# Kernel tuning notes

Hardware: AMD Instinct MI355X
Metric: run time of the kernel (lower is better)

The kernel has to match this reference:

```python
import math
import jax, jax.numpy as jnp
import numpy as np

B, T, C = 2, 2048, 1024
N_HEAD = 16
HEAD_DIM = C // N_HEAD


def setup_inputs() -> dict:
    key = jax.random.key(0)
    k1, k2, k3 = jax.random.split(key, 3)
    x = jax.random.normal(k1, (B, T, C), dtype=jnp.float32)
    w_attn = jax.random.normal(k2, (3 * C, C), dtype=jnp.float32) * 0.02
    w_proj = jax.random.normal(k3, (C, C), dtype=jnp.float32) * 0.02
    return {"x": x, "w_attn": w_attn, "w_proj": w_proj}


def _rope_cos_sin(seq_len, dim, dtype):
    inv_freq = 1.0 / (10000.0 ** (jnp.arange(0, dim, 2, dtype=jnp.float32) / dim))
    t = jnp.arange(seq_len, dtype=jnp.float32)
    freqs = jnp.einsum('i,j->ij', t, inv_freq)          # [T, dim/2]
    emb = jnp.concatenate([freqs, freqs], axis=-1)       # [T, dim]
    return jnp.cos(emb).astype(dtype), jnp.sin(emb).astype(dtype)


def _rotate_half(x):
    x1, x2 = jnp.split(x, 2, axis=-1)
    return jnp.concatenate([-x2, x1], axis=-1)


def _apply_rope(x, cos, sin):
    # x: [B, H, T, D]; cos/sin: [T, D] broadcast over batch/head
    return x * cos[None, None] + _rotate_half(x) * sin[None, None]


def reference(x, w_attn, w_proj):
    b, t, c = x.shape
    h, d = N_HEAD, c // N_HEAD
    qkv = x @ w_attn.T                                   # [B, T, 3C]
    q, k, v = jnp.split(qkv, 3, axis=-1)
    q = q.reshape(b, t, h, d).transpose(0, 2, 1, 3)      # [B, H, T, D]
    k = k.reshape(b, t, h, d).transpose(0, 2, 1, 3)
    v = v.reshape(b, t, h, d).transpose(0, 2, 1, 3)
    cos, sin = _rope_cos_sin(t, d, x.dtype)
    q = _apply_rope(q, cos, sin)
    k = _apply_rope(k, cos, sin)
    logits = jnp.einsum('bhqd,bhkd->bhqk', q, k) * (1.0 / math.sqrt(d))
    causal = jnp.tril(jnp.ones((t, t), dtype=bool))
    logits = jnp.where(causal[None, None], logits, jnp.float32(-jnp.inf).astype(logits.dtype))
    att = jax.nn.softmax(logits, axis=-1)                # [B, H, T, T]
    y = jnp.einsum('bhqk,bhkd->bhqd', att, v)            # [B, H, T, D]
    y = y.transpose(0, 2, 1, 3).reshape(b, t, c)
    return y @ w_proj.T
```

## Files before the change

kernel.cpp:

```cpp
#include <hip/hip_runtime.h>
#include <hip/hip_bf16.h>
#include <math.h>

#define B_ 2
#define T_ 2048
#define C_ 1024
#define H_ 16

typedef __bf16 bf16x8 __attribute__((ext_vector_type(8)));
typedef __bf16 bf16x4 __attribute__((ext_vector_type(4)));
typedef float f32x4 __attribute__((ext_vector_type(4)));
typedef float f32x16 __attribute__((ext_vector_type(16)));
typedef unsigned int u32;

#if __has_builtin(__builtin_amdgcn_exp2f)
#define EXP2(x) __builtin_amdgcn_exp2f(x)
#else
#define EXP2(x) exp2f(x)
#endif

__device__ __forceinline__ void gload16(const void* g, void* l) {
    __builtin_amdgcn_global_load_lds(
        (const __attribute__((address_space(1))) void*)g,
        (__attribute__((address_space(3))) void*)l, 16, 0, 0);
}

__device__ __forceinline__ f32x4 mfma16(bf16x8 a, bf16x8 b, f32x4 c) {
    return __builtin_amdgcn_mfma_f32_16x16x32_bf16(a, b, c, 0, 0, 0);
}
__device__ __forceinline__ f32x16 mfma32(bf16x8 a, bf16x8 b, f32x16 c) {
    return __builtin_amdgcn_mfma_f32_32x32x16_bf16(a, b, c, 0, 0, 0);
}

__device__ __forceinline__ u32 cvtpk(float lo, float hi) {
    u32 r;
    asm("v_cvt_pk_bf16_f32 %0, %1, %2" : "=v"(r) : "v"(lo), "v"(hi));
    return r;
}

__device__ __forceinline__ void plane32swap(u32& a, u32& b) {
#if __has_builtin(__builtin_amdgcn_permlane32_swap)
    auto r = __builtin_amdgcn_permlane32_swap(a, b, false, false);
    a = r[0]; b = r[1];
#else
    asm("v_permlane32_swap_b32 %0, %1" : "+v"(a), "+v"(b));
#endif
}

#define SCLQ 0.18033688011112042f
#define NLOG2_10K_32 (-0.4152410118609203f)

__global__ __launch_bounds__(256) void cast_all(const float* __restrict__ x,
                                                const float* __restrict__ wa,
                                                const float* __restrict__ wp,
                                                __bf16* __restrict__ xb,
                                                __bf16* __restrict__ wab,
                                                __bf16* __restrict__ wpb) {
    const int i = blockIdx.x * 256 + threadIdx.x;
    const float* src;
    __bf16* dst;
    int k;
    if (i < 1048576)               { src = x;  dst = xb;  k = i; }
    else if (i < 1048576 + 786432) { src = wa; dst = wab; k = i - 1048576; }
    else                           { src = wp; dst = wpb; k = i - (1048576 + 786432); }
    float4 v = ((const float4*)src)[k];
    bf16x4 o;
    o[0] = (__bf16)v.x; o[1] = (__bf16)v.y; o[2] = (__bf16)v.z; o[3] = (__bf16)v.w;
    ((bf16x4*)dst)[k] = o;
}

__global__ __launch_bounds__(256) void gemm_qkv(const __bf16* __restrict__ A,
                                                const __bf16* __restrict__ Bw,
                                                __bf16* __restrict__ Qb,
                                                __bf16* __restrict__ Kb,
                                                __bf16* __restrict__ Vt) {
    const int tid  = threadIdx.x;
    const int lane = tid & 63;
    const int w    = tid >> 6;
    const int wr = w >> 1, wc = w & 1;
    const int l15 = lane & 15, lg = lane >> 4;
    const int d0  = blockIdx.y * 24 + blockIdx.x;
    const int xcd = d0 & 7, kk0 = d0 >> 3;
    const int by  = xcd * 4 + (kk0 / 24);
    const int bx  = kk0 % 24;
    const int bm = by * 128, bn = bx * 128;
    const int K = C_;
    __shared__ __bf16 Asm[128 * 64];
    __shared__ __bf16 Bsm[128 * 64];
    f32x4 acc[4][4] = {};

    for (int kt = 0; kt < K; kt += 64) {
        if (kt) __syncthreads();
#pragma unroll
        for (int it = 0; it < 4; ++it) {
            const int c = it * 256 + tid;
            const int row = c >> 3, cc = (c & 7) * 8;
            gload16(A  + (size_t)(bm + row) * K + kt + cc, Asm + c * 8);
            gload16(Bw + (size_t)(bn + row) * K + kt + cc, Bsm + c * 8);
        }
        __syncthreads();
#pragma unroll
        for (int kk = 0; kk < 64; kk += 32) {
            bf16x8 af[4], bf[4];
#pragma unroll
            for (int i = 0; i < 4; ++i)
                af[i] = *(const bf16x8*)&Asm[(wr * 64 + i * 16 + l15) * 64 + kk + lg * 8];
#pragma unroll
            for (int j = 0; j < 4; ++j)
                bf[j] = *(const bf16x8*)&Bsm[(wc * 64 + j * 16 + l15) * 64 + kk + lg * 8];
#pragma unroll
            for (int i = 0; i < 4; ++i)
#pragma unroll
                for (int j = 0; j < 4; ++j)
                    acc[i][j] = mfma16(af[i], bf[j], acc[i][j]);
        }
    }
    const int region  = bn >> 10;
    const int colbase = (bn & 1023) + wc * 64;
    const int h = colbase >> 6;
    if (region < 2) {
        __bf16* dst = region ? Kb : Qb;
        const float scl = region ? 1.0f : SCLQ;
#pragma unroll
        for (int j = 0; j < 2; ++j) {
            const int d = j * 16 + l15;
            const float invf = exp2f((float)d * NLOG2_10K_32);
#pragma unroll
            for (int i = 0; i < 4; ++i)
#pragma unroll
                for (int r = 0; r < 4; ++r) {
                    const int row = bm + wr * 64 + i * 16 + lg * 4 + r;
                    const int b = row >> 11, t = row & (T_ - 1);
                    float sv, cv;
                    __sincosf((float)t * invf, &sv, &cv);
                    const float v1 = acc[i][j][r], v2 = acc[i][j + 2][r];
                    const float o1 = (v1 * cv - v2 * sv) * scl;
                    const float o2 = (v2 * cv + v1 * sv) * scl;
                    const size_t base = ((size_t)(b * H_ + h) * T_ + t) * 64;
                    dst[base + d]      = (__bf16)o1;
                    dst[base + d + 32] = (__bf16)o2;
                }
        }
    } else {
#pragma unroll
        for (int i = 0; i < 4; ++i)
#pragma unroll
            for (int j = 0; j < 4; ++j) {
                const int vcol = colbase + j * 16 + l15;
                const int hh = vcol >> 6, d = vcol & 63;
                const int row0 = bm + wr * 64 + i * 16 + lg * 4;
                const int b = row0 >> 11, t0 = row0 & (T_ - 1);
                u32 dw[2];
                dw[0] = cvtpk(acc[i][j][0], acc[i][j][1]);
                dw[1] = cvtpk(acc[i][j][2], acc[i][j][3]);
                *(uint64_t*)&Vt[((size_t)(b * H_ + hh) * 64 + d) * T_ + t0] =
                    *(uint64_t*)dw;
            }
    }
}

__global__ __launch_bounds__(256) void gemm_proj(const __bf16* __restrict__ A,
                                                 const __bf16* __restrict__ Bw,
                                                 float* __restrict__ Cp,
                                                 int N, int K) {
    const int tid  = threadIdx.x;
    const int lane = tid & 63;
    const int w    = tid >> 6;
    const int wr = w >> 1, wc = w & 1;
    const int l15 = lane & 15, lg = lane >> 4;
    const int d0  = blockIdx.y * 8 + blockIdx.x;
    const int xcd = d0 & 7, kk0 = d0 >> 3;
    const int by  = xcd * 8 + (kk0 >> 3);
    const int bx  = kk0 & 7;
    const int bm = by * 64, bn = bx * 128;
    __shared__ __bf16 Asm[64 * 64];
    __shared__ __bf16 Bsm[128 * 64];
    f32x4 acc[2][4] = {};

    for (int kt = 0; kt < K; kt += 64) {
        if (kt) __syncthreads();
#pragma unroll
        for (int it = 0; it < 2; ++it) {
            const int g = it * 256 + tid;
            const int row = g >> 3, cc = (g & 7) * 8;
            gload16(A + (size_t)(bm + row) * K + kt + cc, Asm + g * 8);
        }
#pragma unroll
        for (int it = 0; it < 4; ++it) {
            const int g = it * 256 + tid;
            const int row = g >> 3, cc = (g & 7) * 8;
            gload16(Bw + (size_t)(bn + row) * K + kt + cc, Bsm + g * 8);
        }
        __syncthreads();
#pragma unroll
        for (int kk = 0; kk < 64; kk += 32) {
            bf16x8 af[2], bf[4];
#pragma unroll
            for (int i = 0; i < 2; ++i)
                af[i] = *(const bf16x8*)&Asm[(wr * 32 + i * 16 + l15) * 64 + kk + lg * 8];
#pragma unroll
            for (int j = 0; j < 4; ++j)
                bf[j] = *(const bf16x8*)&Bsm[(wc * 64 + j * 16 + l15) * 64 + kk + lg * 8];
#pragma unroll
            for (int i = 0; i < 2; ++i)
#pragma unroll
                for (int j = 0; j < 4; ++j)
                    acc[i][j] = mfma16(af[i], bf[j], acc[i][j]);
        }
    }
#pragma unroll
    for (int i = 0; i < 2; ++i)
#pragma unroll
        for (int j = 0; j < 4; ++j)
#pragma unroll
            for (int r = 0; r < 4; ++r) {
                const int row = bm + wr * 32 + i * 16 + lg * 4 + r;
                const int col = bn + wc * 64 + j * 16 + l15;
                Cp[(size_t)row * N + col] = acc[i][j][r];
            }
}

__global__ __launch_bounds__(512, 4) void attn_fwd(const __bf16* __restrict__ Qb,
                                                   const __bf16* __restrict__ Kb,
                                                   const __bf16* __restrict__ Vt,
                                                   __bf16* __restrict__ Yatt) {
    const int gid = blockIdx.x;
    const int bh = (gid & 7) * 4 + ((gid >> 3) & 3);
    const int qq = gid >> 5;
    const int qt = (qq < 8) ? (15 - qq) : (qq - 8);
    const int b = bh >> 4, h = bh & 15;
    const int tid = threadIdx.x, lane = tid & 63, w = tid >> 6;
    const int qgrp = w & 3, kvh = w >> 2;
    const int l31 = lane & 31, hi = lane >> 5;
    const int hi4 = hi * 4;
    __shared__ __bf16 Ksm[2][128 * 64];
    __shared__ __bf16 Vsm[2][64 * 128];

    const int Q0 = qt * 128 + qgrp * 32;
    const int qg = Q0 + l31;
    const __bf16* Qp = Qb + ((size_t)bh * T_ + Q0) * 64;
    const __bf16* Kp = Kb + (size_t)bh * T_ * 64;
    const __bf16* Vp = Vt + (size_t)bh * 64 * T_;

    auto STAGE = [&](int j) {
        __bf16* Ks = Ksm[j & 1];
        __bf16* Vs = Vsm[j & 1];
#pragma unroll
        for (int it = 0; it < 2; ++it) {
            const int g = it * 512 + tid;
            const int kr = g >> 3, kc = (g & 7) ^ (kr & 7);
            gload16(Kp + ((size_t)(j * 128 + kr)) * 64 + kc * 8, Ks + g * 8);
            const int vd = g >> 4, vg = (g & 15) ^ (vd & 15);
            gload16(Vp + (size_t)vd * T_ + j * 128 + vg * 8, Vs + g * 8);
        }
    };

    const int jmax = qt + 1;
    STAGE(0);

    bf16x8 qf[4];
#pragma unroll
    for (int ds = 0; ds < 4; ++ds)
        qf[ds] = *(const bf16x8*)&Qp[l31 * 64 + ds * 16 + hi * 8];

    f32x16 ot[2] = {};
    float l_run = 0.f;

    for (int j = 0; j < jmax; ++j) {
        const int cur = j & 1;
        __builtin_amdgcn_s_barrier();
        if (j + 1 < jmax) {
            STAGE(j + 1);
            asm volatile("s_waitcnt vmcnt(4)" ::: "memory");
        } else {
            asm volatile("s_waitcnt vmcnt(0)" ::: "memory");
        }
        __builtin_amdgcn_s_barrier();
        __builtin_amdgcn_sched_barrier(0);

        if (j * 128 + kvh * 64 <= Q0 + 31) {
            f32x16 st[2] = {};
#pragma unroll
            for (int a = 0; a < 2; ++a)
#pragma unroll
                for (int ds = 0; ds < 4; ++ds) {
                    const int row = kvh * 64 + a * 32 + l31;
                    const int off = (ds * 32 + hi * 16) ^ ((row & 7) << 4);
                    bf16x8 kf = *(const bf16x8*)((const char*)Ksm[cur] + row * 128 + off);
                    st[a] = mfma32(kf, qf[ds], st[a]);
                }
            if (j == qt) {
#pragma unroll
                for (int a = 0; a < 2; ++a)
#pragma unroll
                    for (int r = 0; r < 16; ++r) {
                        const int kv = j * 128 + kvh * 64 + a * 32 +
                                       (r & 3) + 8 * (r >> 2) + hi4;
                        if (kv > qg) st[a][r] = -1e30f;
                    }
            }
            float s0 = 0.f, s1 = 0.f;
#pragma unroll
            for (int a = 0; a < 2; ++a)
#pragma unroll
                for (int r = 0; r < 16; ++r) {
                    const float e = EXP2(st[a][r]);
                    st[a][r] = e;
                    if (r & 1) s1 += e; else s0 += e;
                }
            l_run += s0 + s1;
            bf16x8 pa[4];
#pragma unroll
            for (int ks = 0; ks < 4; ++ks) {
                const int a = ks >> 1, rb = (ks & 1) * 8;
                u32 X0 = cvtpk(st[a][rb + 0], st[a][rb + 1]);
                u32 X1 = cvtpk(st[a][rb + 2], st[a][rb + 3]);
                u32 Y0 = cvtpk(st[a][rb + 4], st[a][rb + 5]);
                u32 Y1 = cvtpk(st[a][rb + 6], st[a][rb + 7]);
                plane32swap(X0, Y0);
                plane32swap(X1, Y1);
                u32 dw[4] = {X0, X1, Y0, Y1};
                pa[ks] = *(bf16x8*)dw;
            }
#pragma unroll
            for (int ks = 0; ks < 4; ++ks)
#pragma unroll
                for (int db = 0; db < 2; ++db) {
                    const int row = db * 32 + l31;
                    const int gnl = (kvh * 8 + ks * 2 + hi) ^ (row & 15);
                    bf16x8 vf = *(const bf16x8*)((const char*)Vsm[cur] +
                                                 row * 256 + gnl * 16);
                    ot[db] = mfma32(vf, pa[ks], ot[db]);
                }
        }
    }
    __builtin_amdgcn_s_barrier();
    f32x4* m4 = (f32x4*)&Ksm[0][0];
    float* lb = (float*)&Vsm[0][0];
    if (w >= 4) {
        const int woff = (w - 4) * 64 + lane;
#pragma unroll
        for (int db = 0; db < 2; ++db)
#pragma unroll
            for (int rq = 0; rq < 4; ++rq) {
                f32x4 v;
                v[0] = ot[db][rq * 4 + 0]; v[1] = ot[db][rq * 4 + 1];
                v[2] = ot[db][rq * 4 + 2]; v[3] = ot[db][rq * 4 + 3];
                m4[(db * 4 + rq) * 256 + woff] = v;
            }
        lb[woff] = l_run;
    }
    __builtin_amdgcn_s_barrier();
    if (w < 4) {
        const int woff = w * 64 + lane;
#pragma unroll
        for (int db = 0; db < 2; ++db)
#pragma unroll
            for (int rq = 0; rq < 4; ++rq) {
                f32x4 v = m4[(db * 4 + rq) * 256 + woff];
                ot[db][rq * 4 + 0] += v[0]; ot[db][rq * 4 + 1] += v[1];
                ot[db][rq * 4 + 2] += v[2]; ot[db][rq * 4 + 3] += v[3];
            }
        l_run += lb[woff];
        l_run += __shfl_xor(l_run, 32);
        const float inv = 1.f / l_run;
        __bf16* Yp = Yatt + ((size_t)(b * T_ + qg)) * C_ + h * 64;
#pragma unroll
        for (int db = 0; db < 2; ++db)
#pragma unroll
            for (int rq = 0; rq < 4; ++rq) {
                const int r = rq * 4;
                u32 dw[2];
                dw[0] = cvtpk(ot[db][r] * inv,     ot[db][r + 1] * inv);
                dw[1] = cvtpk(ot[db][r + 2] * inv, ot[db][r + 3] * inv);
                const int d = db * 32 + 8 * rq + hi4;
                *(uint64_t*)&Yp[d] = *(uint64_t*)dw;
            }
    }
}

extern "C" void kernel_launch(void* const* d_in, const int* in_sizes, int n_in,
                              void* d_out, int out_size, void* d_ws, size_t ws_size,
                              hipStream_t stream) {
    const float* x      = (const float*)d_in[0];
    const float* w_attn = (const float*)d_in[1];
    const float* w_proj = (const float*)d_in[2];
    float* out = (float*)d_out;
    char* ws = (char*)d_ws;

    __bf16* xb  = (__bf16*)(ws);
    __bf16* wab = (__bf16*)(ws + 8388608);
    __bf16* wpb = (__bf16*)(ws + 14680064);
    __bf16* Qb  = (__bf16*)(ws + 16777216);
    __bf16* Kb  = (__bf16*)(ws + 25165824);
    __bf16* Vt  = (__bf16*)(ws + 33554432);
    __bf16* Ya  = (__bf16*)(ws + 41943040);

    cast_all<<<dim3(8192), 256, 0, stream>>>(x, w_attn, w_proj, xb, wab, wpb);

    gemm_qkv<<<dim3(3 * C_ / 128, B_ * T_ / 128), 256, 0, stream>>>(
        xb, wab, Qb, Kb, Vt);

    attn_fwd<<<dim3(16 * 32), 512, 0, stream>>>(Qb, Kb, Vt, Ya);

    gemm_proj<<<dim3(C_ / 128, B_ * T_ / 64), 256, 0, stream>>>(
        Ya, wpb, out, C_, C_);
}
```

Baseline: 99.97 us.

## Swizzle GEMM LDS tiles and use single-buffered 256-wide KV tiles in attention

Both GEMM kernels now XOR-swizzle the 16-byte column groups in shared memory on load and on fragment read, which targets LDS bank conflicts. The attention kernel drops double buffering in favor of one 256-row K/V tile per iteration, halving the number of loop iterations and barriers. Each wave now processes 128 keys per step in four 32-key sub-blocks. The cost is that global loads are no longer overlapped with compute, since each tile is waited on fully before use, and diagonal masking now covers a 256-wide tile.

```diff
diff --git a/kernel.cpp b/kernel.cpp
--- a/kernel.cpp
+++ b/kernel.cpp
@@ -94,20 +94,24 @@
 #pragma unroll
         for (int it = 0; it < 4; ++it) {
             const int c = it * 256 + tid;
-            const int row = c >> 3, cc = (c & 7) * 8;
-            gload16(A  + (size_t)(bm + row) * K + kt + cc, Asm + c * 8);
-            gload16(Bw + (size_t)(bn + row) * K + kt + cc, Bsm + c * 8);
+            const int row = c >> 3, sg = (c & 7) ^ (row & 7);
+            gload16(A  + (size_t)(bm + row) * K + kt + sg * 8, Asm + c * 8);
+            gload16(Bw + (size_t)(bn + row) * K + kt + sg * 8, Bsm + c * 8);
         }
         __syncthreads();
 #pragma unroll
-        for (int kk = 0; kk < 64; kk += 32) {
+        for (int k2 = 0; k2 < 2; ++k2) {
             bf16x8 af[4], bf[4];
 #pragma unroll
-            for (int i = 0; i < 4; ++i)
-                af[i] = *(const bf16x8*)&Asm[(wr * 64 + i * 16 + l15) * 64 + kk + lg * 8];
-#pragma unroll
-            for (int j = 0; j < 4; ++j)
-                bf[j] = *(const bf16x8*)&Bsm[(wc * 64 + j * 16 + l15) * 64 + kk + lg * 8];
+            for (int i = 0; i < 4; ++i) {
+                const int row = wr * 64 + i * 16 + l15;
+                af[i] = *(const bf16x8*)&Asm[row * 64 + (((k2 * 4 + lg) ^ (row & 7)) * 8)];
+            }
+#pragma unroll
+            for (int j = 0; j < 4; ++j) {
+                const int row = wc * 64 + j * 16 + l15;
+                bf[j] = *(const bf16x8*)&Bsm[row * 64 + (((k2 * 4 + lg) ^ (row & 7)) * 8)];
+            }
 #pragma unroll
             for (int i = 0; i < 4; ++i)
 #pragma unroll
@@ -182,25 +186,29 @@
 #pragma unroll
         for (int it = 0; it < 2; ++it) {
             const int g = it * 256 + tid;
-            const int row = g >> 3, cc = (g & 7) * 8;
-            gload16(A + (size_t)(bm + row) * K + kt + cc, Asm + g * 8);
+            const int row = g >> 3, sg = (g & 7) ^ (row & 7);
+            gload16(A + (size_t)(bm + row) * K + kt + sg * 8, Asm + g * 8);
         }
 #pragma unroll
         for (int it = 0; it < 4; ++it) {
             const int g = it * 256 + tid;
-            const int row = g >> 3, cc = (g & 7) * 8;
-            gload16(Bw + (size_t)(bn + row) * K + kt + cc, Bsm + g * 8);
+            const int row = g >> 3, sg = (g & 7) ^ (row & 7);
+            gload16(Bw + (size_t)(bn + row) * K + kt + sg * 8, Bsm + g * 8);
         }
         __syncthreads();
 #pragma unroll
-        for (int kk = 0; kk < 64; kk += 32) {
+        for (int k2 = 0; k2 < 2; ++k2) {
             bf16x8 af[2], bf[4];
 #pragma unroll
-            for (int i = 0; i < 2; ++i)
-                af[i] = *(const bf16x8*)&Asm[(wr * 32 + i * 16 + l15) * 64 + kk + lg * 8];
-#pragma unroll
-            for (int j = 0; j < 4; ++j)
-                bf[j] = *(const bf16x8*)&Bsm[(wc * 64 + j * 16 + l15) * 64 + kk + lg * 8];
+            for (int i = 0; i < 2; ++i) {
+                const int row = wr * 32 + i * 16 + l15;
+                af[i] = *(const bf16x8*)&Asm[row * 64 + (((k2 * 4 + lg) ^ (row & 7)) * 8)];
+            }
+#pragma unroll
+            for (int j = 0; j < 4; ++j) {
+                const int row = wc * 64 + j * 16 + l15;
+                bf[j] = *(const bf16x8*)&Bsm[row * 64 + (((k2 * 4 + lg) ^ (row & 7)) * 8)];
+            }
 #pragma unroll
             for (int i = 0; i < 2; ++i)
 #pragma unroll
@@ -233,8 +241,8 @@
     const int qgrp = w & 3, kvh = w >> 2;
     const int l31 = lane & 31, hi = lane >> 5;
     const int hi4 = hi * 4;
-    __shared__ __bf16 Ksm[2][128 * 64];
-    __shared__ __bf16 Vsm[2][64 * 128];
+    __shared__ __bf16 Ksm[256 * 64];
+    __shared__ __bf16 Vsm[64 * 256];
 
     const int Q0 = qt * 128 + qgrp * 32;
     const int qg = Q0 + l31;
@@ -242,21 +250,16 @@
     const __bf16* Kp = Kb + (size_t)bh * T_ * 64;
     const __bf16* Vp = Vt + (size_t)bh * 64 * T_;
 
-    auto STAGE = [&](int j) {
-        __bf16* Ks = Ksm[j & 1];
-        __bf16* Vs = Vsm[j & 1];
-#pragma unroll
-        for (int it = 0; it < 2; ++it) {
+    auto STAGE = [&](int jt) {
+#pragma unroll
+        for (int it = 0; it < 4; ++it) {
             const int g = it * 512 + tid;
             const int kr = g >> 3, kc = (g & 7) ^ (kr & 7);
-            gload16(Kp + ((size_t)(j * 128 + kr)) * 64 + kc * 8, Ks + g * 8);
-            const int vd = g >> 4, vg = (g & 15) ^ (vd & 15);
-            gload16(Vp + (size_t)vd * T_ + j * 128 + vg * 8, Vs + g * 8);
+            gload16(Kp + ((size_t)(jt * 256 + kr)) * 64 + kc * 8, Ksm + g * 8);
+            const int vd = g >> 5, vg = ((g & 15) ^ (vd & 15)) | (g & 16);
+            gload16(Vp + (size_t)vd * T_ + jt * 256 + vg * 8, Vsm + g * 8);
         }
     };
-
-    const int jmax = qt + 1;
-    STAGE(0);
 
     bf16x8 qf[4];
 #pragma unroll
@@ -266,77 +269,68 @@
     f32x16 ot[2] = {};
     float l_run = 0.f;
 
-    for (int j = 0; j < jmax; ++j) {
-        const int cur = j & 1;
+    const int jmax = (qt >> 1) + 1;
+    for (int jt = 0; jt < jmax; ++jt) {
         __builtin_amdgcn_s_barrier();
-        if (j + 1 < jmax) {
-            STAGE(j + 1);
-            asm volatile("s_waitcnt vmcnt(4)" ::: "memory");
-        } else {
-            asm volatile("s_waitcnt vmcnt(0)" ::: "memory");
-        }
+        STAGE(jt);
+        asm volatile("s_waitcnt vmcnt(0)" ::: "memory");
         __builtin_amdgcn_s_barrier();
         __builtin_amdgcn_sched_barrier(0);
 
-        if (j * 128 + kvh * 64 <= Q0 + 31) {
-            f32x16 st[2] = {};
-#pragma unroll
-            for (int a = 0; a < 2; ++a)
+        if (jt * 256 + kvh * 128 <= Q0 + 31) {
+            const bool diag = (jt == jmax - 1);
+#pragma unroll
+            for (int a = 0; a < 4; ++a) {
+                f32x16 st = {};
 #pragma unroll
                 for (int ds = 0; ds < 4; ++ds) {
-                    const int row = kvh * 64 + a * 32 + l31;
+                    const int row = kvh * 128 + a * 32 + l31;
                     const int off = (ds * 32 + hi * 16) ^ ((row & 7) << 4);
-                    bf16x8 kf = *(const bf16x8*)((const char*)Ksm[cur] + row * 128 + off);
-                    st[a] = mfma32(kf, qf[ds], st[a]);
+                    bf16x8 kf = *(const bf16x8*)((const char*)Ksm + row * 128 + off);
+                    st = mfma32(kf, qf[ds], st);
                 }
-            if (j == qt) {
-#pragma unroll
-                for (int a = 0; a < 2; ++a)
+                if (diag) {
 #pragma unroll
                     for (int r = 0; r < 16; ++r) {
-                        const int kv = j * 128 + kvh * 64 + a * 32 +
+                        const int kv = jt * 256 + kvh * 128 + a * 32 +
                                        (r & 3) + 8 * (r >> 2) + hi4;
-                        if (kv > qg) st[a][r] = -1e30f;
+                        if (kv > qg) st[r] = -1e30f;
                     }
-            }
-            float s0 = 0.f, s1 = 0.f;
-#pragma unroll
-            for (int a = 0; a < 2; ++a)
+                }
+                float s0 = 0.f, s1 = 0.f;
 #pragma unroll
                 for (int r = 0; r < 16; ++r) {
-                    const float e = EXP2(st[a][r]);
-                    st[a][r] = e;
+                    const float e = EXP2(st[r]);
+                    st[r] = e;
                     if (r & 1) s1 += e; else s0 += e;
                 }
-            l_run += s0 + s1;
-            bf16x8 pa[4];
-#pragma unroll
-            for (int ks = 0; ks < 4; ++ks) {
-                const int a = ks >> 1, rb = (ks & 1) * 8;
-                u32 X0 = cvtpk(st[a][rb + 0], st[a][rb + 1]);
-                u32 X1 = cvtpk(st[a][rb + 2], st[a][rb + 3]);
-                u32 Y0 = cvtpk(st[a][rb + 4], st[a][rb + 5]);
-                u32 Y1 = cvtpk(st[a][rb + 6], st[a][rb + 7]);
-                plane32swap(X0, Y0);
-                plane32swap(X1, Y1);
-                u32 dw[4] = {X0, X1, Y0, Y1};
-                pa[ks] = *(bf16x8*)dw;
-            }
-#pragma unroll
-            for (int ks = 0; ks < 4; ++ks)
+                l_run += s0 + s1;
+                u32 X0 = cvtpk(st[0], st[1]),  X1 = cvtpk(st[2], st[3]);
+                u32 Y0 = cvtpk(st[4], st[5]),  Y1 = cvtpk(st[6], st[7]);
+                plane32swap(X0, Y0); plane32swap(X1, Y1);
+                u32 dw0[4] = {X0, X1, Y0, Y1};
+                bf16x8 pa0 = *(bf16x8*)dw0;
+                u32 Z0 = cvtpk(st[8], st[9]),   Z1 = cvtpk(st[10], st[11]);
+                u32 W0 = cvtpk(st[12], st[13]), W1 = cvtpk(st[14], st[15]);
+                plane32swap(Z0, W0); plane32swap(Z1, W1);
+                u32 dw1[4] = {Z0, Z1, W0, W1};
+                bf16x8 pa1 = *(bf16x8*)dw1;
 #pragma unroll
                 for (int db = 0; db < 2; ++db) {
                     const int row = db * 32 + l31;
-                    const int gnl = (kvh * 8 + ks * 2 + hi) ^ (row & 15);
-                    bf16x8 vf = *(const bf16x8*)((const char*)Vsm[cur] +
-                                                 row * 256 + gnl * 16);
-                    ot[db] = mfma32(vf, pa[ks], ot[db]);
+                    const int g0 = (kvh * 16) | ((4 * a + hi)     ^ (row & 15));
+                    const int g1 = (kvh * 16) | ((4 * a + 2 + hi) ^ (row & 15));
+                    bf16x8 v0 = *(const bf16x8*)((const char*)Vsm + row * 512 + g0 * 16);
+                    bf16x8 v1 = *(const bf16x8*)((const char*)Vsm + row * 512 + g1 * 16);
+                    ot[db] = mfma32(v0, pa0, ot[db]);
+                    ot[db] = mfma32(v1, pa1, ot[db]);
                 }
+            }
         }
     }
     __builtin_amdgcn_s_barrier();
-    f32x4* m4 = (f32x4*)&Ksm[0][0];
-    float* lb = (float*)&Vsm[0][0];
+    f32x4* m4 = (f32x4*)&Ksm[0];
+    float* lb = (float*)&Vsm[0];
     if (w >= 4) {
         const int woff = (w - 4) * 64 + lane;
 #pragma unroll
```

New measurement: 108.7 us. 1.09x slower.
